# Kernel tuning notes

Hardware: AMD Instinct MI355X
Metric: run time of the kernel (lower is better)

Reference implementation:

```python
import jax, jax.numpy as jnp
import numpy as np

N_NODES = 50000
N_EDGES = 600000
DIM = 128
K = 3
N_LAYERS = 3
LEAKY_SLOPE = 0.01  # nn.LeakyReLU default
RE_NORM = 1.0       # 2/lambda_max with lambda_max=2 (standard ChebNet approximation)


def setup_inputs() -> dict:
    key = jax.random.key(0)
    ks = jax.random.split(key, 8)
    weights = jax.random.normal(ks[0], (N_NODES,), dtype=jnp.float32)
    src = jax.random.randint(ks[1], (N_EDGES,), 0, N_NODES)
    dst = jax.random.randint(ks[2], (N_EDGES,), 0, N_NODES)
    lin_in_w = jax.random.normal(ks[3], (1, DIM), dtype=jnp.float32) * 0.5
    lin_in_b = jnp.zeros((DIM,), dtype=jnp.float32)
    cheb_ws = jax.random.normal(ks[4], (N_LAYERS, K * DIM, DIM), dtype=jnp.float32) * 0.05
    cheb_bs = jnp.zeros((N_LAYERS, DIM), dtype=jnp.float32)
    pred_w = jax.random.normal(ks[5], (DIM, 1), dtype=jnp.float32) * 0.05
    pred_b = jnp.zeros((1,), dtype=jnp.float32)
    return {"weights": weights, "src": src, "dst": dst,
            "lin_in_w": lin_in_w, "lin_in_b": lin_in_b,
            "cheb_ws": cheb_ws, "cheb_bs": cheb_bs,
            "pred_w": pred_w, "pred_b": pred_b}


def _cheb_conv(x, W, b, src, dst, d_invsqrt, n):
    # DGL ChebConv with lambda_max=2 -> re_norm=1: scaled Laplacian L_hat = -D^-1/2 A D^-1/2
    def spmm(f):  # unnormalized Laplacian-style aggregation: D^-1/2 A D^-1/2 f
        h = f * d_invsqrt
        agg = jax.ops.segment_sum(h[src], dst, num_segments=n)
        return agg * d_invsqrt

    X0 = x
    terms = [X0]
    h = spmm(X0)
    X1 = -RE_NORM * h + X0 * (RE_NORM - 1.0)
    terms.append(X1)
    for _ in range(2, K):
        h = spmm(X1)
        Xi = -2.0 * RE_NORM * h + X1 * (2.0 * (RE_NORM - 1.0)) - X0
        terms.append(Xi)
        X0, X1 = X1, Xi
    Xt = jnp.concatenate(terms, axis=1)  # [N, K*DIM]
    return jax.nn.relu(Xt @ W + b)       # DGL ChebConv default activation=F.relu


def reference(weights, src, dst, lin_in_w, lin_in_b, cheb_ws, cheb_bs, pred_w, pred_b):
    n = weights.shape[0]
    # dgl.add_self_loop
    loop = jnp.arange(n, dtype=src.dtype)
    src_f = jnp.concatenate([src, loop])
    dst_f = jnp.concatenate([dst, loop])
    # in-degree normalization D^-1/2 (clamp min 1)
    deg = jax.ops.segment_sum(jnp.ones_like(dst_f, dtype=jnp.float32), dst_f, num_segments=n)
    d_invsqrt = jnp.power(jnp.clip(deg, 1.0), -0.5)[:, None]  # [N,1]

    feat = weights[:, None] @ lin_in_w + lin_in_b             # [N, DIM]
    emb = _cheb_conv(feat, cheb_ws[0], cheb_bs[0], src_f, dst_f, d_invsqrt, n)
    for i in range(1, N_LAYERS):
        emb = jax.nn.leaky_relu(emb, negative_slope=LEAKY_SLOPE)
        emb = _cheb_conv(emb, cheb_ws[i], cheb_bs[i], src_f, dst_f, d_invsqrt, n)
    logits = emb @ pred_w + pred_b                            # do_train=True path
    return logits
```

## Files before the change

kernel.cpp:

```cpp
#include <hip/hip_runtime.h>

typedef unsigned int uint;
typedef unsigned short ushort;

#define NN 50000
#define NE 600000
#define DIM 128
#define KD 384
#define PADK 40

typedef __attribute__((ext_vector_type(8))) short short8;
typedef __attribute__((ext_vector_type(4))) float float4v;

static __device__ __forceinline__ ushort f2b(float f) {
    uint u = __float_as_uint(f);
    return (ushort)((u + 0x7FFFu + ((u >> 16) & 1u)) >> 16);
}
static __device__ __forceinline__ float blo(uint u) { return __uint_as_float(u << 16); }
static __device__ __forceinline__ float bhi(uint u) { return __uint_as_float(u & 0xFFFF0000u); }

__global__ void k_init(int* __restrict__ cnt, const float* __restrict__ cw,
                       ushort* __restrict__ wt) {
    if (blockIdx.x < 49) {
        int i = blockIdx.x * 256 + threadIdx.x;
        if (i < 12544) ((int4*)cnt)[i] = make_int4(0, 0, 0, 0);
    } else {
        int i = (blockIdx.x - 49) * 256 + threadIdx.x;
        if (i < 3 * KD * DIM) {
            int l = i / (KD * DIM), rem = i - l * (KD * DIM);
            int k = rem >> 7, n = rem & 127;
            wt[(size_t)l * KD * DIM + (size_t)n * KD + k] = f2b(cw[i]);
        }
    }
}

__global__ void k_hist(const int* __restrict__ dst, int* __restrict__ cnt) {
    int e = blockIdx.x * 256 + threadIdx.x;
    if (e < NE) atomicAdd(&cnt[dst[e]], 1);
}

__global__ __launch_bounds__(256) void k_scan1(const int* __restrict__ cnt,
                                               int* __restrict__ incl,
                                               int* __restrict__ bsums,
                                               float* __restrict__ dinv) {
    __shared__ int sh[256];
    int i = blockIdx.x * 256 + threadIdx.x;
    int v = (i < NN) ? cnt[i] : 0;
    if (i < NN) dinv[i] = rsqrtf((float)(v + 1));
    sh[threadIdx.x] = v;
    __syncthreads();
    for (int d = 1; d < 256; d <<= 1) {
        int t = (threadIdx.x >= d) ? sh[threadIdx.x - d] : 0;
        __syncthreads();
        sh[threadIdx.x] += t;
        __syncthreads();
    }
    incl[i] = sh[threadIdx.x];
    if (threadIdx.x == 255) bsums[blockIdx.x] = sh[255];
}

__global__ __launch_bounds__(256) void k_scan3(const int* __restrict__ cnt,
                                               int* __restrict__ incl_cursor,
                                               const int* __restrict__ bsums,
                                               int* __restrict__ offs) {
    __shared__ int sh[256];
    __shared__ int boff;
    int tid = threadIdx.x;
    int v = (tid < 196) ? bsums[tid] : 0;
    sh[tid] = v;
    __syncthreads();
    for (int d = 1; d < 256; d <<= 1) {
        int t = (tid >= d) ? sh[tid - d] : 0;
        __syncthreads();
        sh[tid] += t;
        __syncthreads();
    }
    if (tid == blockIdx.x) boff = sh[tid] - v;
    __syncthreads();
    int i = blockIdx.x * 256 + tid;
    if (i >= NN) return;
    int excl = incl_cursor[i] - cnt[i] + boff;
    offs[i] = excl;
    incl_cursor[i] = excl;
    if (i == NN - 1) offs[NN] = NE;
}

__global__ void k_fill(const int* __restrict__ src, const int* __restrict__ dst,
                       int* __restrict__ cursor, const float* __restrict__ dinv,
                       const float* __restrict__ w_in,
                       uint2* __restrict__ csrE, float* __restrict__ hw) {
    int e = blockIdx.x * 256 + threadIdx.x;
    if (e < NE) {
        int s = src[e], d = dst[e];
        int p = atomicAdd(&cursor[d], 1);
        float ds = dinv[s];
        uint2 rec;
        rec.x = (uint)s;
        rec.y = __float_as_uint(ds * dinv[d]);
        csrE[p] = rec;
        hw[p] = ds * w_in[s];
    }
}

__global__ __launch_bounds__(256) void k_uv(
        const float* __restrict__ lw, const float* __restrict__ lb,
        const float* __restrict__ cw, float* __restrict__ uv) {
    __shared__ float swv[128], sbv[128];
    int tid = threadIdx.x;
    if (tid < 128) { swv[tid] = lw[tid]; sbv[tid] = lb[tid]; }
    __syncthreads();
    for (int idx = tid; idx < 768; idx += 256) {
        int vec = idx >> 7, c = idx & 127;
        int t = vec >> 1;
        const float* coef = (vec & 1) ? sbv : swv;
        float s = 0.f;
        for (int k = 0; k < 128; ++k)
            s += coef[k] * cw[(size_t)(t * 128 + k) * 128 + c];
        uv[idx] = s;
    }
}

__global__ __launch_bounds__(256) void k_spmv1(
        const int* __restrict__ offs, const uint2* __restrict__ csrE,
        const float* __restrict__ hw, const float* __restrict__ dinv,
        const float* __restrict__ w, float2* __restrict__ SS) {
    int n = blockIdx.x * 16 + (threadIdx.x >> 4);
    int l = threadIdx.x & 15;
    int j0 = offs[n], j1 = offs[n + 1];
    float sA = 0.f, sB = 0.f;
    const float* ew = (const float*)csrE;
    for (int j = j0 + l; j < j1; j += 16) {
        sA += hw[j];
        sB += ew[2 * j + 1];
    }
#pragma unroll
    for (int off = 8; off > 0; off >>= 1) {
        sA += __shfl_down(sA, off, 16);
        sB += __shfl_down(sB, off, 16);
    }
    if (l == 0) {
        float dn = dinv[n], id = dn * dn;
        float2 o;
        o.x = dn * sA + id * w[n];
        o.y = sB + id;
        SS[n] = o;
    }
}

__global__ __launch_bounds__(256) void k_spmv2(
        const int* __restrict__ offs, const uint2* __restrict__ csrE,
        const float2* __restrict__ SS, const float* __restrict__ dinv,
        float2* __restrict__ SS2) {
    int n = blockIdx.x * 16 + (threadIdx.x >> 4);
    int l = threadIdx.x & 15;
    int j0 = offs[n], j1 = offs[n + 1];
    float sC = 0.f, sD = 0.f;
    for (int j = j0 + l; j < j1; j += 16) {
        uint2 e = csrE[j];
        float wv = __uint_as_float(e.y);
        float2 s = SS[e.x];
        sC = fmaf(wv, s.x, sC);
        sD = fmaf(wv, s.y, sD);
    }
#pragma unroll
    for (int off = 8; off > 0; off >>= 1) {
        sC += __shfl_down(sC, off, 16);
        sD += __shfl_down(sD, off, 16);
    }
    if (l == 0) {
        float dn = dinv[n], id = dn * dn;
        float2 s = SS[n];
        float2 o;
        o.x = sC + id * s.x;
        o.y = sD + id * s.y;
        SS2[n] = o;
    }
}

__global__ __launch_bounds__(256) void k_l1out(
        const float* __restrict__ w, const float2* __restrict__ SS,
        const float2* __restrict__ SS2, const float* __restrict__ uv,
        const float* __restrict__ bias, ushort* __restrict__ Pb) {
    int n = blockIdx.x * 4 + (threadIdx.x >> 6);
    int l = threadIdx.x & 63;
    float a0 = w[n];
    float2 s1 = SS[n], s2 = SS2[n];
    float a1 = -s1.x, b1 = -s1.y;
    float a2 = 2.f * s2.x - a0, b2 = 2.f * s2.y - 1.f;
    const float2* uv2 = (const float2*)uv;
    float2 u0 = uv2[l],       v0 = uv2[64 + l];
    float2 u1 = uv2[128 + l], v1 = uv2[192 + l];
    float2 u2 = uv2[256 + l], v2 = uv2[320 + l];
    float2 bb = ((const float2*)bias)[l];
    float o0 = bb.x + a0 * u0.x + v0.x + a1 * u1.x + b1 * v1.x + a2 * u2.x + b2 * v2.x;
    float o1 = bb.y + a0 * u0.y + v0.y + a1 * u1.y + b1 * v1.y + a2 * u2.y + b2 * v2.y;
    ushort2 o;
    o.x = f2b(fmaxf(o0, 0.f));
    o.y = f2b(fmaxf(o1, 0.f));
    ((ushort2*)(Pb + (size_t)n * DIM))[l] = o;
}

__global__ __launch_bounds__(256) void k_gather1(
        const ushort* __restrict__ Xb, const int* __restrict__ offs,
        const uint2* __restrict__ csrE, const float* __restrict__ dinv,
        ushort* __restrict__ Qb) {
    int n = __builtin_amdgcn_readfirstlane(blockIdx.x * 4 + (threadIdx.x >> 6));
    int lane = threadIdx.x & 63;
    int j0 = offs[n], j1 = offs[n + 1];
    const uint* Xu = (const uint*)Xb;
    float a0 = 0.f, a1 = 0.f;
#pragma unroll 4
    for (int j = j0; j < j1; ++j) {
        uint2 e = csrE[j];
        float wv = __uint_as_float(e.y);
        uint u = Xu[(size_t)e.x * 64 + lane];
        a0 = fmaf(wv, blo(u), a0);
        a1 = fmaf(wv, bhi(u), a1);
    }
    float dn = dinv[n];
    float id = dn * dn;
    uint un = Xu[(size_t)n * 64 + lane];
    uint ow = (uint)f2b(-(a0 + blo(un) * id))
            | ((uint)f2b(-(a1 + bhi(un) * id)) << 16);
    ((uint*)Qb)[(size_t)n * 64 + lane] = ow;
}

__global__ __launch_bounds__(256) void k_gather2(
        const ushort* __restrict__ X1b, const ushort* __restrict__ X0b,
        const int* __restrict__ offs, const uint2* __restrict__ csrE,
        const float* __restrict__ dinv, ushort* __restrict__ Rb) {
    int n = __builtin_amdgcn_readfirstlane(blockIdx.x * 4 + (threadIdx.x >> 6));
    int lane = threadIdx.x & 63;
    int j0 = offs[n], j1 = offs[n + 1];
    const uint* Xu = (const uint*)X1b;
    float a0 = 0.f, a1 = 0.f;
#pragma unroll 4
    for (int j = j0; j < j1; ++j) {
        uint2 e = csrE[j];
        float wv = __uint_as_float(e.y);
        uint u = Xu[(size_t)e.x * 64 + lane];
        a0 = fmaf(wv, blo(u), a0);
        a1 = fmaf(wv, bhi(u), a1);
    }
    float dn = dinv[n];
    float id = dn * dn;
    uint u1n = Xu[(size_t)n * 64 + lane];
    uint u0n = ((const uint*)X0b)[(size_t)n * 64 + lane];
    uint ow = (uint)f2b(-2.f * (a0 + blo(u1n) * id) - blo(u0n))
            | ((uint)f2b(-2.f * (a1 + bhi(u1n) * id) - bhi(u0n)) << 16);
    ((uint*)Rb)[(size_t)n * 64 + lane] = ow;
}

__global__ __launch_bounds__(256) void k_gemm(
        const ushort* __restrict__ X0b, const ushort* __restrict__ X1b,
        const ushort* __restrict__ X2b, const ushort* __restrict__ Wt,
        const float* __restrict__ bias, ushort* __restrict__ outb) {
    __shared__ ushort As[128 * PADK];
    __shared__ ushort Bs[128 * PADK];
    int tid = threadIdx.x;
    int nbase = blockIdx.x * 128;
    int wave = tid >> 6, lane = tid & 63;
    int wr = wave >> 1, wc = wave & 1;
    int l15 = lane & 15, quad = lane >> 4;

    float4v acc[4][4];
#pragma unroll
    for (int i = 0; i < 4; ++i)
#pragma unroll
        for (int j = 0; j < 4; ++j) acc[i][j] = (float4v)0.f;

    int srow = tid >> 1, shalf = tid & 1;
    int gm = nbase + srow; if (gm >= NN) gm = NN - 1;

    for (int c = 0; c < 12; ++c) {
        int part = c >> 2;
        int k0 = (c & 3) * 32;
        const ushort* Xp = (part == 0) ? X0b : ((part == 1) ? X1b : X2b);
        const uint4* ga = (const uint4*)(Xp + (size_t)gm * DIM + k0 + shalf * 16);
        uint4 a0 = ga[0], a1 = ga[1];
        const uint4* gb = (const uint4*)(Wt + (size_t)srow * KD + c * 32 + shalf * 16);
        uint4 b0 = gb[0], b1 = gb[1];
        __syncthreads();
        uint4* pa = (uint4*)(As + srow * PADK + shalf * 16);
        pa[0] = a0; pa[1] = a1;
        uint4* pb = (uint4*)(Bs + srow * PADK + shalf * 16);
        pb[0] = b0; pb[1] = b1;
        __syncthreads();
        short8 af[4], bf[4];
#pragma unroll
        for (int i = 0; i < 4; ++i) {
            af[i] = *(const short8*)(As + (wr * 64 + i * 16 + l15) * PADK + quad * 8);
            bf[i] = *(const short8*)(Bs + (wc * 64 + i * 16 + l15) * PADK + quad * 8);
        }
#pragma unroll
        for (int i = 0; i < 4; ++i)
#pragma unroll
            for (int j = 0; j < 4; ++j)
                acc[i][j] = __builtin_amdgcn_mfma_f32_16x16x32_bf16(
                    af[i], bf[j], acc[i][j], 0, 0, 0);
    }

    float bv[4];
#pragma unroll
    for (int j = 0; j < 4; ++j) bv[j] = bias[wc * 64 + j * 16 + l15];
#pragma unroll
    for (int i = 0; i < 4; ++i) {
#pragma unroll
        for (int r = 0; r < 4; ++r) {
            int node = nbase + wr * 64 + i * 16 + quad * 4 + r;
            if (node < NN) {
#pragma unroll
                for (int j = 0; j < 4; ++j) {
                    int col = wc * 64 + j * 16 + l15;
                    outb[(size_t)node * DIM + col] =
                        f2b(fmaxf(acc[i][j][r] + bv[j], 0.f));
                }
            }
        }
    }
}

__global__ __launch_bounds__(256) void k_gemm_pred(
        const ushort* __restrict__ X0b, const ushort* __restrict__ X1b,
        const ushort* __restrict__ X2b, const ushort* __restrict__ Wt,
        const float* __restrict__ bias, const float* __restrict__ pw,
        const float* __restrict__ pb, float* __restrict__ logits) {
    __shared__ ushort As[128 * PADK];
    __shared__ ushort Bs[128 * PADK];
    __shared__ float lsum[128];
    int tid = threadIdx.x;
    int nbase = blockIdx.x * 128;
    int wave = tid >> 6, lane = tid & 63;
    int wr = wave >> 1, wc = wave & 1;
    int l15 = lane & 15, quad = lane >> 4;

    float4v acc[4][4];
#pragma unroll
    for (int i = 0; i < 4; ++i)
#pragma unroll
        for (int j = 0; j < 4; ++j) acc[i][j] = (float4v)0.f;

    int srow = tid >> 1, shalf = tid & 1;
    int gm = nbase + srow; if (gm >= NN) gm = NN - 1;

    for (int c = 0; c < 12; ++c) {
        int part = c >> 2;
        int k0 = (c & 3) * 32;
        const ushort* Xp = (part == 0) ? X0b : ((part == 1) ? X1b : X2b);
        const uint4* ga = (const uint4*)(Xp + (size_t)gm * DIM + k0 + shalf * 16);
        uint4 a0 = ga[0], a1 = ga[1];
        const uint4* gb = (const uint4*)(Wt + (size_t)srow * KD + c * 32 + shalf * 16);
        uint4 b0 = gb[0], b1 = gb[1];
        __syncthreads();
        uint4* pa = (uint4*)(As + srow * PADK + shalf * 16);
        pa[0] = a0; pa[1] = a1;
        uint4* pb2 = (uint4*)(Bs + srow * PADK + shalf * 16);
        pb2[0] = b0; pb2[1] = b1;
        __syncthreads();
        short8 af[4], bf[4];
#pragma unroll
        for (int i = 0; i < 4; ++i) {
            af[i] = *(const short8*)(As + (wr * 64 + i * 16 + l15) * PADK + quad * 8);
            bf[i] = *(const short8*)(Bs + (wc * 64 + i * 16 + l15) * PADK + quad * 8);
        }
#pragma unroll
        for (int i = 0; i < 4; ++i)
#pragma unroll
            for (int j = 0; j < 4; ++j)
                acc[i][j] = __builtin_amdgcn_mfma_f32_16x16x32_bf16(
                    af[i], bf[j], acc[i][j], 0, 0, 0);
    }

    __syncthreads();
    if (tid < 128) lsum[tid] = 0.f;
    __syncthreads();
    float bv[4], pwv[4];
#pragma unroll
    for (int j = 0; j < 4; ++j) {
        int col = wc * 64 + j * 16 + l15;
        bv[j] = bias[col];
        pwv[j] = pw[col];
    }
#pragma unroll
    for (int i = 0; i < 4; ++i) {
#pragma unroll
        for (int r = 0; r < 4; ++r) {
            float local = 0.f;
#pragma unroll
            for (int j = 0; j < 4; ++j)
                local = fmaf(fmaxf(acc[i][j][r] + bv[j], 0.f), pwv[j], local);
            local += __shfl_xor(local, 1, 64);
            local += __shfl_xor(local, 2, 64);
            local += __shfl_xor(local, 4, 64);
            local += __shfl_xor(local, 8, 64);
            if (l15 == 0)
                atomicAdd(&lsum[wr * 64 + i * 16 + quad * 4 + r], local);
        }
    }
    __syncthreads();
    if (tid < 128) {
        int node = nbase + tid;
        if (node < NN) logits[node] = lsum[tid] + pb[0];
    }
}

extern "C" void kernel_launch(void* const* d_in, const int* in_sizes, int n_in,
                              void* d_out, int out_size, void* d_ws, size_t ws_size,
                              hipStream_t stream) {
    int i_weights = 0, i_src = 1, i_dst = 2, i_lw = 3, i_lb = 4,
        i_cw = 5, i_cb = 6, i_pw = 7, i_pb = 8;
    {
        int seen600k = 0, seen128 = 0;
        for (int i = 0; i < n_in; ++i) {
            int s = in_sizes[i];
            if (s == 50000) i_weights = i;
            else if (s == 600000) { if (seen600k == 0) i_src = i; else i_dst = i; ++seen600k; }
            else if (s == 128) { if (seen128 == 0) i_lw = i; else if (seen128 == 1) i_lb = i; else i_pw = i; ++seen128; }
            else if (s == 147456) i_cw = i;
            else if (s == 384) i_cb = i;
            else if (s == 1) i_pb = i;
        }
    }
    const float* weights = (const float*)d_in[i_weights];
    const int*   src     = (const int*)d_in[i_src];
    const int*   dst     = (const int*)d_in[i_dst];
    const float* lin_w   = (const float*)d_in[i_lw];
    const float* lin_b   = (const float*)d_in[i_lb];
    const float* cheb_w  = (const float*)d_in[i_cw];
    const float* cheb_b  = (const float*)d_in[i_cb];
    const float* pred_w  = (const float*)d_in[i_pw];
    const float* pred_b  = (const float*)d_in[i_pb];
    float* out = (float*)d_out;

    float*  ws      = (float*)d_ws;
    float*  dinv    = ws;
    int*    offs    = (int*)(ws + 50048);
    int*    cnt     = offs + 50056;
    int*    incl    = cnt + 50176;
    int*    bsums   = incl + 50176;
    uint2*  csrE    = (uint2*)(bsums + 256);
    float*  hw      = (float*)(csrE + NE);
    float2* SS      = (float2*)(hw + NE);
    float2* SS2     = SS + 50048;
    float*  uv      = (float*)(SS2 + 50048);
    ushort* Pb      = (ushort*)(uv + 768);
    ushort* Qb      = Pb + (size_t)NN * DIM;
    ushort* Rb      = Qb + (size_t)NN * DIM;
    ushort* Wtb     = Rb + (size_t)NN * DIM;

    k_init<<<625, 256, 0, stream>>>(cnt, cheb_w, Wtb);
    k_hist<<<2344, 256, 0, stream>>>(dst, cnt);
    k_scan1<<<196, 256, 0, stream>>>(cnt, incl, bsums, dinv);
    k_scan3<<<196, 256, 0, stream>>>(cnt, incl, bsums, offs);
    k_fill<<<2344, 256, 0, stream>>>(src, dst, incl, dinv, weights, csrE, hw);

    k_uv<<<1, 256, 0, stream>>>(lin_w, lin_b, cheb_w, uv);
    k_spmv1<<<3125, 256, 0, stream>>>(offs, csrE, hw, dinv, weights, SS);
    k_spmv2<<<3125, 256, 0, stream>>>(offs, csrE, SS, dinv, SS2);
    k_l1out<<<12500, 256, 0, stream>>>(weights, SS, SS2, uv, cheb_b, Pb);

    k_gather1<<<12500, 256, 0, stream>>>(Pb, offs, csrE, dinv, Qb);
    k_gather2<<<12500, 256, 0, stream>>>(Qb, Pb, offs, csrE, dinv, Rb);
    k_gemm<<<391, 256, 0, stream>>>(Pb, Qb, Rb, Wtb + (size_t)KD * DIM,
                                    cheb_b + DIM, Pb);
    k_gather1<<<12500, 256, 0, stream>>>(Pb, offs, csrE, dinv, Qb);
    k_gather2<<<12500, 256, 0, stream>>>(Qb, Pb, offs, csrE, dinv, Rb);
    k_gemm_pred<<<391, 256, 0, stream>>>(Pb, Qb, Rb, Wtb + (size_t)2 * KD * DIM,
                                         cheb_b + 2 * DIM, pred_w, pred_b, out);
}
```

Before: 342.0 us.

## Chunk node features into 16-column slabs and gather per chunk with edge-parallel lanes

```diff
diff --git a/kernel.cpp b/kernel.cpp
--- a/kernel.cpp
+++ b/kernel.cpp
@@ -2,12 +2,15 @@
 
 typedef unsigned int uint;
 typedef unsigned short ushort;
+typedef unsigned long long ulong64;
 
 #define NN 50000
 #define NE 600000
 #define DIM 128
 #define KD 384
 #define PADK 40
+#define CH 8
+#define CHS ((size_t)NN * 16)
 
 typedef __attribute__((ext_vector_type(8))) short short8;
 typedef __attribute__((ext_vector_type(4))) float float4v;
@@ -197,58 +200,97 @@
     ushort2 o;
     o.x = f2b(fmaxf(o0, 0.f));
     o.y = f2b(fmaxf(o1, 0.f));
-    ((ushort2*)(Pb + (size_t)n * DIM))[l] = o;
-}
-
-__global__ __launch_bounds__(256) void k_gather1(
-        const ushort* __restrict__ Xb, const int* __restrict__ offs,
+    ((ushort2*)Pb)[(size_t)(l >> 3) * (NN * 8) + (size_t)n * 8 + (l & 7)] = o;
+}
+
+__global__ __launch_bounds__(256, 8) void k_gather1c(
+        const ushort* __restrict__ Xc, const int* __restrict__ offs,
         const uint2* __restrict__ csrE, const float* __restrict__ dinv,
-        ushort* __restrict__ Qb) {
-    int n = __builtin_amdgcn_readfirstlane(blockIdx.x * 4 + (threadIdx.x >> 6));
-    int lane = threadIdx.x & 63;
-    int j0 = offs[n], j1 = offs[n + 1];
-    const uint* Xu = (const uint*)Xb;
-    float a0 = 0.f, a1 = 0.f;
-#pragma unroll 4
-    for (int j = j0; j < j1; ++j) {
-        uint2 e = csrE[j];
-        float wv = __uint_as_float(e.y);
-        uint u = Xu[(size_t)e.x * 64 + lane];
-        a0 = fmaf(wv, blo(u), a0);
-        a1 = fmaf(wv, bhi(u), a1);
-    }
-    float dn = dinv[n];
-    float id = dn * dn;
-    uint un = Xu[(size_t)n * 64 + lane];
-    uint ow = (uint)f2b(-(a0 + blo(un) * id))
-            | ((uint)f2b(-(a1 + bhi(un) * id)) << 16);
-    ((uint*)Qb)[(size_t)n * 64 + lane] = ow;
-}
-
-__global__ __launch_bounds__(256) void k_gather2(
-        const ushort* __restrict__ X1b, const ushort* __restrict__ X0b,
+        ushort* __restrict__ Qc) {
+    int chunk = blockIdx.x & 7;
+    int wave = threadIdx.x >> 6, lane = threadIdx.x & 63;
+    int eslot = lane >> 3, dw = lane & 7;
+    const uint* Xu = (const uint*)(Xc + (size_t)chunk * CHS);
+    uint* Qu = (uint*)(Qc + (size_t)chunk * CHS);
+    const int ngroups = (NN + 31) / 32;
+    for (int g = blockIdx.x >> 3; g < ngroups; g += 256) {
+        int n0 = g * 32 + wave * 8;
+#pragma unroll 1
+        for (int nn = 0; nn < 8; ++nn) {
+            int n = n0 + nn;
+            if (n >= NN) break;
+            int j0 = offs[n], j1 = offs[n + 1];
+            float a0 = 0.f, a1 = 0.f;
+            for (int j = j0; j < j1; j += 8) {
+                int jj = j + eslot;
+                float wv = 0.f; uint u = 0;
+                if (jj < j1) {
+                    ulong64 ev = __builtin_nontemporal_load(
+                        (const ulong64*)&csrE[jj]);
+                    wv = __uint_as_float((uint)(ev >> 32));
+                    u = Xu[(size_t)(uint)ev * 8 + dw];
+                }
+                a0 = fmaf(wv, blo(u), a0);
+                a1 = fmaf(wv, bhi(u), a1);
+            }
+            a0 += __shfl_xor(a0, 8, 64);  a1 += __shfl_xor(a1, 8, 64);
+            a0 += __shfl_xor(a0, 16, 64); a1 += __shfl_xor(a1, 16, 64);
+            a0 += __shfl_xor(a0, 32, 64); a1 += __shfl_xor(a1, 32, 64);
+            if (eslot == 0) {
+                float dn = dinv[n], id = dn * dn;
+                uint un = Xu[(size_t)n * 8 + dw];
+                uint ow = (uint)f2b(-(a0 + blo(un) * id))
+                        | ((uint)f2b(-(a1 + bhi(un) * id)) << 16);
+                Qu[(size_t)n * 8 + dw] = ow;
+            }
+        }
+    }
+}
+
+__global__ __launch_bounds__(256, 8) void k_gather2c(
+        const ushort* __restrict__ X1c, const ushort* __restrict__ X0c,
         const int* __restrict__ offs, const uint2* __restrict__ csrE,
-        const float* __restrict__ dinv, ushort* __restrict__ Rb) {
-    int n = __builtin_amdgcn_readfirstlane(blockIdx.x * 4 + (threadIdx.x >> 6));
-    int lane = threadIdx.x & 63;
-    int j0 = offs[n], j1 = offs[n + 1];
-    const uint* Xu = (const uint*)X1b;
-    float a0 = 0.f, a1 = 0.f;
-#pragma unroll 4
-    for (int j = j0; j < j1; ++j) {
-        uint2 e = csrE[j];
-        float wv = __uint_as_float(e.y);
-        uint u = Xu[(size_t)e.x * 64 + lane];
-        a0 = fmaf(wv, blo(u), a0);
-        a1 = fmaf(wv, bhi(u), a1);
-    }
-    float dn = dinv[n];
-    float id = dn * dn;
-    uint u1n = Xu[(size_t)n * 64 + lane];
-    uint u0n = ((const uint*)X0b)[(size_t)n * 64 + lane];
-    uint ow = (uint)f2b(-2.f * (a0 + blo(u1n) * id) - blo(u0n))
-            | ((uint)f2b(-2.f * (a1 + bhi(u1n) * id) - bhi(u0n)) << 16);
-    ((uint*)Rb)[(size_t)n * 64 + lane] = ow;
+        const float* __restrict__ dinv, ushort* __restrict__ Rc) {
+    int chunk = blockIdx.x & 7;
+    int wave = threadIdx.x >> 6, lane = threadIdx.x & 63;
+    int eslot = lane >> 3, dw = lane & 7;
+    const uint* Xu = (const uint*)(X1c + (size_t)chunk * CHS);
+    const uint* X0u = (const uint*)(X0c + (size_t)chunk * CHS);
+    uint* Ru = (uint*)(Rc + (size_t)chunk * CHS);
+    const int ngroups = (NN + 31) / 32;
+    for (int g = blockIdx.x >> 3; g < ngroups; g += 256) {
+        int n0 = g * 32 + wave * 8;
+#pragma unroll 1
+        for (int nn = 0; nn < 8; ++nn) {
+            int n = n0 + nn;
+            if (n >= NN) break;
+            int j0 = offs[n], j1 = offs[n + 1];
+            float a0 = 0.f, a1 = 0.f;
+            for (int j = j0; j < j1; j += 8) {
+                int jj = j + eslot;
+                float wv = 0.f; uint u = 0;
+                if (jj < j1) {
+                    ulong64 ev = __builtin_nontemporal_load(
+                        (const ulong64*)&csrE[jj]);
+                    wv = __uint_as_float((uint)(ev >> 32));
+                    u = Xu[(size_t)(uint)ev * 8 + dw];
+                }
+                a0 = fmaf(wv, blo(u), a0);
+                a1 = fmaf(wv, bhi(u), a1);
+            }
+            a0 += __shfl_xor(a0, 8, 64);  a1 += __shfl_xor(a1, 8, 64);
+            a0 += __shfl_xor(a0, 16, 64); a1 += __shfl_xor(a1, 16, 64);
+            a0 += __shfl_xor(a0, 32, 64); a1 += __shfl_xor(a1, 32, 64);
+            if (eslot == 0) {
+                float dn = dinv[n], id = dn * dn;
+                uint u1n = Xu[(size_t)n * 8 + dw];
+                uint u0n = X0u[(size_t)n * 8 + dw];
+                uint ow = (uint)f2b(-2.f * (a0 + blo(u1n) * id) - blo(u0n))
+                        | ((uint)f2b(-2.f * (a1 + bhi(u1n) * id) - bhi(u0n)) << 16);
+                Ru[(size_t)n * 8 + dw] = ow;
+            }
+        }
+    }
 }
 
 __global__ __launch_bounds__(256) void k_gemm(
@@ -274,9 +316,9 @@
 
     for (int c = 0; c < 12; ++c) {
         int part = c >> 2;
-        int k0 = (c & 3) * 32;
+        int cki = (c & 3) * 2 + shalf;
         const ushort* Xp = (part == 0) ? X0b : ((part == 1) ? X1b : X2b);
-        const uint4* ga = (const uint4*)(Xp + (size_t)gm * DIM + k0 + shalf * 16);
+        const uint4* ga = (const uint4*)(Xp + (size_t)cki * CHS + (size_t)gm * 16);
         uint4 a0 = ga[0], a1 = ga[1];
         const uint4* gb = (const uint4*)(Wt + (size_t)srow * KD + c * 32 + shalf * 16);
         uint4 b0 = gb[0], b1 = gb[1];
@@ -311,8 +353,7 @@
             if (node < NN) {
 #pragma unroll
                 for (int j = 0; j < 4; ++j) {
-                    int col = wc * 64 + j * 16 + l15;
-                    outb[(size_t)node * DIM + col] =
+                    outb[(size_t)(wc * 4 + j) * CHS + (size_t)node * 16 + l15] =
                         f2b(fmaxf(acc[i][j][r] + bv[j], 0.f));
                 }
             }
@@ -345,9 +386,9 @@
 
     for (int c = 0; c < 12; ++c) {
         int part = c >> 2;
-        int k0 = (c & 3) * 32;
+        int cki = (c & 3) * 2 + shalf;
         const ushort* Xp = (part == 0) ? X0b : ((part == 1) ? X1b : X2b);
-        const uint4* ga = (const uint4*)(Xp + (size_t)gm * DIM + k0 + shalf * 16);
+        const uint4* ga = (const uint4*)(Xp + (size_t)cki * CHS + (size_t)gm * 16);
         uint4 a0 = ga[0], a1 = ga[1];
         const uint4* gb = (const uint4*)(Wt + (size_t)srow * KD + c * 32 + shalf * 16);
         uint4 b0 = gb[0], b1 = gb[1];
@@ -459,12 +500,12 @@
     k_spmv2<<<3125, 256, 0, stream>>>(offs, csrE, SS, dinv, SS2);
     k_l1out<<<12500, 256, 0, stream>>>(weights, SS, SS2, uv, cheb_b, Pb);
 
-    k_gather1<<<12500, 256, 0, stream>>>(Pb, offs, csrE, dinv, Qb);
-    k_gather2<<<12500, 256, 0, stream>>>(Qb, Pb, offs, csrE, dinv, Rb);
+    k_gather1c<<<2048, 256, 0, stream>>>(Pb, offs, csrE, dinv, Qb);
+    k_gather2c<<<2048, 256, 0, stream>>>(Qb, Pb, offs, csrE, dinv, Rb);
     k_gemm<<<391, 256, 0, stream>>>(Pb, Qb, Rb, Wtb + (size_t)KD * DIM,
                                     cheb_b + DIM, Pb);
-    k_gather1<<<12500, 256, 0, stream>>>(Pb, offs, csrE, dinv, Qb);
-    k_gather2<<<12500, 256, 0, stream>>>(Qb, Pb, offs, csrE, dinv, Rb);
+    k_gather1c<<<2048, 256, 0, stream>>>(Pb, offs, csrE, dinv, Qb);
+    k_gather2c<<<2048, 256, 0, stream>>>(Qb, Pb, offs, csrE, dinv, Rb);
     k_gemm_pred<<<391, 256, 0, stream>>>(Pb, Qb, Rb, Wtb + (size_t)2 * KD * DIM,
                                          cheb_b + 2 * DIM, pred_w, pred_b, out);
 }
```

Measured after the change: 798.5 us. 2.34x slower.
